# Kernel optimization log

Measured on AMD Instinct MI355X. Metric: run time of the kernel, lower is better.

Reference implementation:

```python
import jax, jax.numpy as jnp
import numpy as np

B, S, D, H, F = 2, 2048, 2048, 16, 8192
EPS = 1e-6


def _layernorm(x, g, b):
    # torch: mean/std over last dim, std is Bessel-corrected (unbiased), divide by (std + eps)
    m = jnp.mean(x, axis=-1, keepdims=True)
    s = jnp.std(x, axis=-1, keepdims=True, ddof=1)
    return g * (x - m) / (s + EPS) + b


def setup_inputs() -> dict:
    key = jax.random.key(0)
    ks = jax.random.split(key, 16)
    w = lambda k, shape, s=0.02: (jax.random.normal(k, shape, jnp.float32) * s)
    return {
        "x": jax.random.normal(ks[0], (B, S, D), jnp.float32),
        "mask": jnp.ones((1, 1, S, S), jnp.int32),
        "wq": w(ks[1], (D, D)), "bq": jnp.zeros((D,), jnp.float32),
        "wk": w(ks[2], (D, D)), "bk": jnp.zeros((D,), jnp.float32),
        "wv": w(ks[3], (D, D)), "bv": jnp.zeros((D,), jnp.float32),
        "wo": w(ks[4], (D, D)), "bo": jnp.zeros((D,), jnp.float32),
        "w1": w(ks[5], (D, F)), "b1": jnp.zeros((F,), jnp.float32),
        "w2": w(ks[6], (F, D)), "b2": jnp.zeros((D,), jnp.float32),
        "ln1_g": jnp.ones((D,), jnp.float32), "ln1_b": jnp.zeros((D,), jnp.float32),
        "ln2_g": jnp.ones((D,), jnp.float32), "ln2_b": jnp.zeros((D,), jnp.float32),
    }


def reference(x, mask, wq, bq, wk, bk, wv, bv, wo, bo, w1, b1, w2, b2, ln1_g, ln1_b, ln2_g, ln2_b):
    Bx, Sx, Dx = x.shape
    dk = Dx // H
    # --- self-attention sublayer (pre-norm residual) ---
    n = _layernorm(x, ln1_g, ln1_b)
    q = (n @ wq + bq).reshape(Bx, Sx, H, dk)
    k = (n @ wk + bk).reshape(Bx, Sx, H, dk)
    v = (n @ wv + bv).reshape(Bx, Sx, H, dk)
    scores = jnp.einsum('bqhd,bkhd->bhqk', q, k) / jnp.sqrt(jnp.float32(dk))
    scores = jnp.where(mask == 0, jnp.float32(-1e9), scores)
    attn = jax.nn.softmax(scores, axis=-1)  # [B,H,S,S]
    o = jnp.einsum('bhqk,bkhd->bqhd', attn, v).reshape(Bx, Sx, Dx)
    x = x + (o @ wo + bo)
    # --- feed-forward sublayer (pre-norm residual) ---
    n2 = _layernorm(x, ln2_g, ln2_b)
    x = x + (jax.nn.relu(n2 @ w1 + b1) @ w2 + b2)
    return x
```

## Files before the change

### kernel.cpp

```cpp
#include <hip/hip_runtime.h>
#include <hip/hip_bf16.h>
#include <cmath>

#define BB  2
#define SS  2048
#define DD  2048
#define HH  16
#define DKK 128
#define FF  8192
#define FQ  2048
#define MM  4096
#define EPSL 1e-6f

typedef __attribute__((ext_vector_type(8))) short  short8;
typedef __attribute__((ext_vector_type(4))) float  floatx4;
typedef __hip_bfloat16 bf16t;

__device__ __forceinline__ float bits2f(ushort u) {
    return __uint_as_float(((unsigned int)u) << 16);
}
__device__ __forceinline__ ushort f2bits(float f) {
    __hip_bfloat16 h = __float2bfloat16(f);
    return *reinterpret_cast<ushort*>(&h);
}

__global__ __launch_bounds__(256) void ln_kernel(const void* __restrict__ x,
                                                 const float* __restrict__ g,
                                                 const float* __restrict__ b,
                                                 bf16t* __restrict__ out,
                                                 int in_f32) {
    const int row = blockIdx.x;
    const int t = threadIdx.x;

    float v[8];
    if (in_f32) {
        const float* xr = (const float*)x + (size_t)row * DD;
        const float4 a4 = ((const float4*)xr)[2 * t];
        const float4 b4 = ((const float4*)xr)[2 * t + 1];
        v[0] = a4.x; v[1] = a4.y; v[2] = a4.z; v[3] = a4.w;
        v[4] = b4.x; v[5] = b4.y; v[6] = b4.z; v[7] = b4.w;
    } else {
        const ushort* xr = (const ushort*)x + (size_t)row * DD;
        union { uint4 u; ushort s[8]; } p;
        p.u = ((const uint4*)xr)[t];
#pragma unroll
        for (int i = 0; i < 8; i++) v[i] = bits2f(p.s[i]);
    }

    float sum = 0.f, sq = 0.f;
#pragma unroll
    for (int i = 0; i < 8; i++) { sum += v[i]; sq += v[i] * v[i]; }
#pragma unroll
    for (int off = 32; off > 0; off >>= 1) {
        sum += __shfl_down(sum, off);
        sq  += __shfl_down(sq, off);
    }
    __shared__ float ssum[4], ssq[4];
    const int wid = t >> 6, lane = t & 63;
    if (lane == 0) { ssum[wid] = sum; ssq[wid] = sq; }
    __syncthreads();
    if (t == 0) {
        float S = 0.f, Q = 0.f;
#pragma unroll
        for (int i = 0; i < 4; i++) { S += ssum[i]; Q += ssq[i]; }
        ssum[0] = S; ssq[0] = Q;
    }
    __syncthreads();
    const float S = ssum[0], Q = ssq[0];
    const float mean = S / (float)DD;
    float var = (Q - S * mean) / (float)(DD - 1);
    var = fmaxf(var, 0.f);
    const float inv = 1.0f / (sqrtf(var) + EPSL);

    const float4 ga = ((const float4*)g)[2 * t], gb = ((const float4*)g)[2 * t + 1];
    const float4 ba = ((const float4*)b)[2 * t], bb4 = ((const float4*)b)[2 * t + 1];
    const float gv[8] = {ga.x, ga.y, ga.z, ga.w, gb.x, gb.y, gb.z, gb.w};
    const float bv[8] = {ba.x, ba.y, ba.z, ba.w, bb4.x, bb4.y, bb4.z, bb4.w};

    union { uint4 u; ushort s[8]; } o;
#pragma unroll
    for (int i = 0; i < 8; i++) o.s[i] = f2bits((v[i] - mean) * inv * gv[i] + bv[i]);
    ((uint4*)((ushort*)out + (size_t)row * DD))[t] = o.u;
}

__global__ __launch_bounds__(256) void wtrans_kernel(const float* __restrict__ in,
                                                     bf16t* __restrict__ out,
                                                     int Cs, int r0, int c0, int nR) {
    __shared__ ushort tile[32][33];
    const int tx = threadIdx.x, ty = threadIdx.y;
    const int cc = blockIdx.x * 32, rr = blockIdx.y * 32;
#pragma unroll
    for (int j = 0; j < 4; j++)
        tile[ty + j * 8][tx] = f2bits(in[(size_t)(r0 + rr + ty + j * 8) * Cs + c0 + cc + tx]);
    __syncthreads();
    ushort* op = (ushort*)out;
#pragma unroll
    for (int j = 0; j < 4; j++)
        op[(size_t)(cc + ty + j * 8) * nR + rr + tx] = tile[tx][ty + j * 8];
}

__global__ __launch_bounds__(256) void gemm_bt(const bf16t* __restrict__ A,
                                               const bf16t* __restrict__ BT,
                                               const float* __restrict__ bias,
                                               const void* __restrict__ residual, int res_mode,
                                               void* __restrict__ C, int c_f32,
                                               int Nx, int Kx, int relu, int vt) {
    __shared__ __align__(16) ushort At[128 * 32];
    __shared__ __align__(16) ushort Bt[128 * 32];

    const int tid = threadIdx.x;
    const int wid = tid >> 6, lane = tid & 63;
    const int m16 = lane & 15, quad = lane >> 4;
    const int wr = wid >> 1, wc = wid & 1;
    const int m0 = blockIdx.y * 128, n0 = blockIdx.x * 128;

    floatx4 acc[4][4];
#pragma unroll
    for (int i = 0; i < 4; i++)
#pragma unroll
        for (int j = 0; j < 4; j++) acc[i][j] = (floatx4){0.f, 0.f, 0.f, 0.f};

    const int rc = lane >> 2, c8 = (lane & 3) * 8;
    const ushort* gA0 = (const ushort*)A  + (size_t)(m0 + rc) * Kx + c8;
    const ushort* gB0 = (const ushort*)BT + (size_t)(n0 + rc) * Kx + c8;

    const int nk = Kx / 32;
    for (int kt = 0; kt < nk; kt++) {
        __syncthreads();
#pragma unroll
        for (int cc = 0; cc < 2; cc++) {
            const int ch = wid * 2 + cc;
            const ushort* ga = gA0 + (size_t)(ch * 16) * Kx + kt * 32;
            const ushort* gb = gB0 + (size_t)(ch * 16) * Kx + kt * 32;
            __builtin_amdgcn_global_load_lds(
                (const __attribute__((address_space(1))) void*)ga,
                (__attribute__((address_space(3))) void*)(&At[ch * 512]), 16, 0, 0);
            __builtin_amdgcn_global_load_lds(
                (const __attribute__((address_space(1))) void*)gb,
                (__attribute__((address_space(3))) void*)(&Bt[ch * 512]), 16, 0, 0);
        }
        __syncthreads();

        short8 af[4], bfr[4];
#pragma unroll
        for (int i = 0; i < 4; i++)
            af[i] = *(const short8*)&At[(wr * 64 + i * 16 + m16) * 32 + quad * 8];
#pragma unroll
        for (int j = 0; j < 4; j++)
            bfr[j] = *(const short8*)&Bt[(wc * 64 + j * 16 + m16) * 32 + quad * 8];
#pragma unroll
        for (int i = 0; i < 4; i++)
#pragma unroll
            for (int j = 0; j < 4; j++)
                acc[i][j] = __builtin_amdgcn_mfma_f32_16x16x32_bf16(af[i], bfr[j], acc[i][j], 0, 0, 0);
    }

#pragma unroll
    for (int i = 0; i < 4; i++) {
        const int row = m0 + wr * 64 + i * 16 + quad * 4;
#pragma unroll
        for (int j = 0; j < 4; j++) {
            const int col = n0 + wc * 64 + j * 16 + m16;
            const float bb = bias ? bias[col] : 0.f;
#pragma unroll
            for (int r = 0; r < 4; r++) {
                float v = acc[i][j][r] + bb;
                if (vt) {
                    const int bb2 = (row + r) >> 11, s = (row + r) & 2047;
                    const int hh2 = col >> 7, dd2 = col & 127;
                    ((ushort*)C)[((size_t)(bb2 * HH + hh2) * DKK + dd2) * SS + s] = f2bits(v);
                } else {
                    const size_t idx = (size_t)(row + r) * Nx + col;
                    if (res_mode == 1)      v += ((const float*)residual)[idx];
                    else if (res_mode == 2) v += bits2f(((const ushort*)residual)[idx]);
                    if (relu) v = fmaxf(v, 0.f);
                    if (c_f32) ((float*)C)[idx] = v;
                    else       ((ushort*)C)[idx] = f2bits(v);
                }
            }
        }
    }
}

#define SQK 144
#define SV  72
#define SP  72
__global__ __launch_bounds__(256) void attn_kernel(const bf16t* __restrict__ q,
                                                   const bf16t* __restrict__ k,
                                                   const bf16t* __restrict__ vT,
                                                   bf16t* __restrict__ o) {
    __shared__ __align__(16) ushort Qt[64 * SQK];
    __shared__ __align__(16) ushort Kt[64 * SQK];
    __shared__ __align__(16) ushort Vt[128 * SV];
    __shared__ __align__(16) ushort Pt[4][16 * SP];

    const int tid = threadIdx.x;
    const int wid = tid >> 6, lane = tid & 63;
    const int m16 = lane & 15, quad = lane >> 4;
    const int qt = blockIdx.x, h = blockIdx.y, b = blockIdx.z;
    const int q0 = qt * 64;

    const ushort* qu = (const ushort*)q;
    const ushort* ku = (const ushort*)k;
    const ushort* vu = (const ushort*)vT;

#pragma unroll
    for (int it = 0; it < 4; it++) {
        const int c0 = tid + it * 256;
        const int r = c0 >> 4, cc = (c0 & 15) * 8;
        *(uint4*)&Qt[r * SQK + cc] =
            *(const uint4*)(qu + (size_t)(b * SS + q0 + r) * DD + h * DKK + cc);
    }

    float m_r[4], l_r[4];
    floatx4 acc_o[8];
#pragma unroll
    for (int r = 0; r < 4; r++) { m_r[r] = -1e30f; l_r[r] = 0.f; }
#pragma unroll
    for (int t = 0; t < 8; t++) acc_o[t] = (floatx4){0.f, 0.f, 0.f, 0.f};

    const float scale = 0.08838834764831845f;

    for (int kt2 = 0; kt2 < SS / 64; kt2++) {
        __syncthreads();
#pragma unroll
        for (int it = 0; it < 4; it++) {
            const int c0 = tid + it * 256;
            const int r = c0 >> 4, cc = (c0 & 15) * 8;
            *(uint4*)&Kt[r * SQK + cc] =
                *(const uint4*)(ku + (size_t)(b * SS + kt2 * 64 + r) * DD + h * DKK + cc);
            const int r2 = c0 >> 3, cc2 = (c0 & 7) * 8;
            *(uint4*)&Vt[r2 * SV + cc2] =
                *(const uint4*)(vu + (size_t)((b * HH + h) * DKK + r2) * SS + kt2 * 64 + cc2);
        }
        __syncthreads();

        short8 af[4];
#pragma unroll
        for (int kk = 0; kk < 4; kk++)
            af[kk] = *(const short8*)&Qt[(wid * 16 + m16) * SQK + kk * 32 + quad * 8];
        floatx4 sacc[4];
#pragma unroll
        for (int j = 0; j < 4; j++) {
            sacc[j] = (floatx4){0.f, 0.f, 0.f, 0.f};
#pragma unroll
            for (int kk = 0; kk < 4; kk++) {
                short8 bfk = *(const short8*)&Kt[(j * 16 + m16) * SQK + kk * 32 + quad * 8];
                sacc[j] = __builtin_amdgcn_mfma_f32_16x16x32_bf16(af[kk], bfk, sacc[j], 0, 0, 0);
            }
        }
#pragma unroll
        for (int r = 0; r < 4; r++) {
            float s0 = sacc[0][r] * scale, s1 = sacc[1][r] * scale;
            float s2 = sacc[2][r] * scale, s3 = sacc[3][r] * scale;
            float mx = fmaxf(fmaxf(s0, s1), fmaxf(s2, s3));
#pragma unroll
            for (int off = 1; off < 16; off <<= 1) mx = fmaxf(mx, __shfl_xor(mx, off));
            const float mnew = fmaxf(m_r[r], mx);
            const float alpha = __expf(m_r[r] - mnew);
            m_r[r] = mnew;
            const float p0 = __expf(s0 - mnew), p1 = __expf(s1 - mnew);
            const float p2 = __expf(s2 - mnew), p3 = __expf(s3 - mnew);
            float rs = p0 + p1 + p2 + p3;
#pragma unroll
            for (int off = 1; off < 16; off <<= 1) rs += __shfl_xor(rs, off);
            l_r[r] = l_r[r] * alpha + rs;
#pragma unroll
            for (int t = 0; t < 8; t++) acc_o[t][r] *= alpha;
            const int prow = (quad * 4 + r) * SP;
            Pt[wid][prow + 0 * 16 + m16] = f2bits(p0);
            Pt[wid][prow + 1 * 16 + m16] = f2bits(p1);
            Pt[wid][prow + 2 * 16 + m16] = f2bits(p2);
            Pt[wid][prow + 3 * 16 + m16] = f2bits(p3);
        }
#pragma unroll
        for (int kk2 = 0; kk2 < 2; kk2++) {
            short8 ap = *(const short8*)&Pt[wid][m16 * SP + kk2 * 32 + quad * 8];
#pragma unroll
            for (int t = 0; t < 8; t++) {
                short8 bv = *(const short8*)&Vt[(t * 16 + m16) * SV + kk2 * 32 + quad * 8];
                acc_o[t] = __builtin_amdgcn_mfma_f32_16x16x32_bf16(ap, bv, acc_o[t], 0, 0, 0);
            }
        }
    }

    ushort* ou = (ushort*)o;
#pragma unroll
    for (int t = 0; t < 8; t++) {
#pragma unroll
        for (int r = 0; r < 4; r++) {
            const float v = acc_o[t][r] / l_r[r];
            ou[(size_t)(b * SS + q0 + wid * 16 + quad * 4 + r) * DD + h * DKK + t * 16 + m16] = f2bits(v);
        }
    }
}

extern "C" void kernel_launch(void* const* d_in, const int* in_sizes, int n_in,
                              void* d_out, int out_size, void* d_ws, size_t ws_size,
                              hipStream_t stream) {
    const float* x   = (const float*)d_in[0];
    const float* wq = (const float*)d_in[2];  const float* bq = (const float*)d_in[3];
    const float* wk = (const float*)d_in[4];  const float* bk = (const float*)d_in[5];
    const float* wv = (const float*)d_in[6];  const float* bv = (const float*)d_in[7];
    const float* wo = (const float*)d_in[8];  const float* bo = (const float*)d_in[9];
    const float* w1 = (const float*)d_in[10]; const float* b1 = (const float*)d_in[11];
    const float* w2 = (const float*)d_in[12]; const float* b2 = (const float*)d_in[13];
    const float* g1 = (const float*)d_in[14]; const float* lb1 = (const float*)d_in[15];
    const float* g2 = (const float*)d_in[16]; const float* lb2 = (const float*)d_in[17];

    char* ws = (char*)d_ws;
    bf16t* S0 = (bf16t*)(ws);
    bf16t* S1 = (bf16t*)(ws + (16u << 20));
    bf16t* S2 = (bf16t*)(ws + (32u << 20));
    bf16t* S3 = (bf16t*)(ws + (48u << 20));
    bf16t* S2b = (bf16t*)(ws + (32u << 20) + (8u << 20));

    bf16t* n_buf  = S0;
    bf16t* k_buf  = S1;
    bf16t* wT_buf = S2;
    bf16t* vT_buf = S3;
    bf16t* q_buf  = (bf16t*)d_out;
    bf16t* a_buf  = S2;
    bf16t* woT    = S0;
    bf16t* x1_buf = S1;
    bf16t* n2_buf = S0;
    bf16t* w1Tq   = S2;
    bf16t* w2Tq   = S2b;
    bf16t* h_buf  = S3;

    const dim3 tb(32, 8);
    const dim3 grT(DD / 32, DD / 32);
    const dim3 grDD(DD / 128, MM / 128);

    ln_kernel<<<MM, 256, 0, stream>>>(x, g1, lb1, n_buf, 1);

    wtrans_kernel<<<grT, tb, 0, stream>>>(wq, wT_buf, DD, 0, 0, DD);
    gemm_bt<<<grDD, 256, 0, stream>>>(n_buf, wT_buf, bq, nullptr, 0, q_buf, 0, DD, DD, 0, 0);
    wtrans_kernel<<<grT, tb, 0, stream>>>(wk, wT_buf, DD, 0, 0, DD);
    gemm_bt<<<grDD, 256, 0, stream>>>(n_buf, wT_buf, bk, nullptr, 0, k_buf, 0, DD, DD, 0, 0);
    wtrans_kernel<<<grT, tb, 0, stream>>>(wv, wT_buf, DD, 0, 0, DD);
    gemm_bt<<<grDD, 256, 0, stream>>>(n_buf, wT_buf, bv, nullptr, 0, vT_buf, 0, DD, DD, 0, 1);

    attn_kernel<<<dim3(SS / 64, HH, BB), 256, 0, stream>>>(q_buf, k_buf, vT_buf, a_buf);

    wtrans_kernel<<<grT, tb, 0, stream>>>(wo, woT, DD, 0, 0, DD);
    gemm_bt<<<grDD, 256, 0, stream>>>(a_buf, woT, bo, x, 1, x1_buf, 0, DD, DD, 0, 0);

    ln_kernel<<<MM, 256, 0, stream>>>(x1_buf, g2, lb2, n2_buf, 0);

    for (int qtr = 0; qtr < 4; qtr++) {
        const int f0 = qtr * FQ;
        wtrans_kernel<<<dim3(FQ / 32, DD / 32), tb, 0, stream>>>(w1, w1Tq, FF, 0, f0, DD);
        gemm_bt<<<dim3(FQ / 128, MM / 128), 256, 0, stream>>>(
            n2_buf, w1Tq, b1 + f0, nullptr, 0, h_buf, 0, FQ, DD, 1, 0);
        wtrans_kernel<<<dim3(DD / 32, FQ / 32), tb, 0, stream>>>(w2, w2Tq, DD, f0, 0, FQ);
        gemm_bt<<<grDD, 256, 0, stream>>>(
            h_buf, w2Tq, qtr == 0 ? b2 : nullptr,
            qtr == 0 ? (const void*)x1_buf : (const void*)d_out, qtr == 0 ? 2 : 1,
            d_out, 1, DD, FQ, 0, 0);
    }
}
```

Before: 1.265 ms.

## Replace 128x128 GEMM with double-buffered 256x256 swizzled-LDS kernel, fuse K/V projections

Replaces the 128x128-tile, single-buffered GEMM with a 512-thread 256x256-tile kernel. It uses K=64 steps, XOR-swizzled LDS layout, double-buffered async global-to-LDS staging interleaved across eight MFMA phases, and raised wave priority around the MFMAs. It also fuses the K and V projections into one launch over a 4096-wide concatenated weight, keeps the residual stream in fp32 in the output buffer, and splits the FFN into halves instead of quarters. The aim is more data reuse per tile and overlap of loads with math, at the cost of higher register and LDS use. The larger tiles also produce fewer blocks per launch, which may underfill the GPU.

```diff
diff --git a/kernel.cpp b/kernel.cpp
--- a/kernel.cpp
+++ b/kernel.cpp
@@ -8,7 +8,7 @@
 #define HH  16
 #define DKK 128
 #define FF  8192
-#define FQ  2048
+#define FH  4096
 #define MM  4096
 #define EPSL 1e-6f
 
@@ -99,78 +99,137 @@
         op[(size_t)(cc + ty + j * 8) * nR + rr + tx] = tile[tx][ty + j * 8];
 }
 
-__global__ __launch_bounds__(256) void gemm_bt(const bf16t* __restrict__ A,
-                                               const bf16t* __restrict__ BT,
-                                               const float* __restrict__ bias,
-                                               const void* __restrict__ residual, int res_mode,
-                                               void* __restrict__ C, int c_f32,
-                                               int Nx, int Kx, int relu, int vt) {
-    __shared__ __align__(16) ushort At[128 * 32];
-    __shared__ __align__(16) ushort Bt[128 * 32];
+template<int IB>
+__device__ __forceinline__ void stage_half(const ushort* __restrict__ g, int Kx,
+                                           ushort* lds, int h, int wid, int lane) {
+#pragma unroll
+    for (int l = 0; l < 2; l++) {
+        const int c = wid * 2 + l;
+        const int rs = (IB == 6) ? (((c & 8) ? 128 : 0) + h * 64 + (c & 7) * 8)
+                                 : ((c >> 2) * 64 + h * 32 + (c & 3) * 8);
+        const int row = rs + (lane >> 3);
+        const int colb = ((lane & 7) * 16) ^ (((row >> 2) & 3) << 5);
+        const ushort* gp = g + (size_t)row * Kx + (colb >> 1);
+        __builtin_amdgcn_global_load_lds(
+            (const __attribute__((address_space(1))) void*)gp,
+            (__attribute__((address_space(3))) void*)(lds + rs * 64), 16, 0, 0);
+    }
+}
+
+#define VMCNT4 asm volatile("s_waitcnt vmcnt(4)" ::: "memory")
+#define VMCNT0 asm volatile("s_waitcnt vmcnt(0)" ::: "memory")
+
+#define STGA(buf, kt, h) stage_half<6>(gAu + (size_t)(kt) * 64, Kx, &LAf[(buf) * (256 * 64)], (h), wid, lane)
+#define STGB(buf, kt, h) stage_half<5>(gBu + (size_t)(kt) * 64, Kx, &LBf[(buf) * (256 * 64)], (h), wid, lane)
+
+#define PHASE(BUF, MH, NH, STAGE_STMT, WAIT_STMT)                                   \
+    do {                                                                            \
+        const ushort* LAc = &LAf[(BUF) * (256 * 64)];                               \
+        const ushort* LBc = &LBf[(BUF) * (256 * 64)];                               \
+        short8 af[4][2], bfr[2][2];                                                 \
+        _Pragma("unroll") for (int i = 0; i < 4; i++) {                             \
+            const int ar = arow0 + ((MH) * 4 + i) * 16;                             \
+            af[i][0] = *(const short8*)&LAc[ar * 64 + swz0];                        \
+            af[i][1] = *(const short8*)&LAc[ar * 64 + swz1];                        \
+        }                                                                           \
+        _Pragma("unroll") for (int j = 0; j < 2; j++) {                             \
+            const int br = brow0 + ((NH) * 2 + j) * 16;                             \
+            bfr[j][0] = *(const short8*)&LBc[br * 64 + swz0];                       \
+            bfr[j][1] = *(const short8*)&LBc[br * 64 + swz1];                       \
+        }                                                                           \
+        STAGE_STMT;                                                                 \
+        asm volatile("s_waitcnt lgkmcnt(8)" ::: "memory");                          \
+        __builtin_amdgcn_s_barrier();                                               \
+        asm volatile("s_waitcnt lgkmcnt(0)" ::: "memory");                          \
+        __builtin_amdgcn_s_setprio(1);                                              \
+        _Pragma("unroll") for (int i = 0; i < 4; i++)                               \
+            _Pragma("unroll") for (int j = 0; j < 2; j++) {                         \
+                acc[(MH) * 4 + i][(NH) * 2 + j] =                                   \
+                    __builtin_amdgcn_mfma_f32_16x16x32_bf16(                        \
+                        af[i][0], bfr[j][0], acc[(MH) * 4 + i][(NH) * 2 + j], 0, 0, 0); \
+                acc[(MH) * 4 + i][(NH) * 2 + j] =                                   \
+                    __builtin_amdgcn_mfma_f32_16x16x32_bf16(                        \
+                        af[i][1], bfr[j][1], acc[(MH) * 4 + i][(NH) * 2 + j], 0, 0, 0); \
+            }                                                                       \
+        __builtin_amdgcn_s_setprio(0);                                              \
+        WAIT_STMT;                                                                  \
+        __builtin_amdgcn_s_barrier();                                               \
+    } while (0)
+
+__global__ __launch_bounds__(512, 2) void gemm256(const bf16t* __restrict__ A,
+                                                  const bf16t* __restrict__ BT,
+                                                  const float* __restrict__ bias,
+                                                  const float* __restrict__ bias2,
+                                                  const void* __restrict__ residual, int res_mode,
+                                                  void* __restrict__ C, void* __restrict__ C2,
+                                                  int c_f32, int Nx, int Kx,
+                                                  int relu, int out_mode) {
+    __shared__ __align__(16) ushort LAf[2 * 256 * 64];
+    __shared__ __align__(16) ushort LBf[2 * 256 * 64];
 
     const int tid = threadIdx.x;
     const int wid = tid >> 6, lane = tid & 63;
     const int m16 = lane & 15, quad = lane >> 4;
-    const int wr = wid >> 1, wc = wid & 1;
-    const int m0 = blockIdx.y * 128, n0 = blockIdx.x * 128;
-
-    floatx4 acc[4][4];
-#pragma unroll
-    for (int i = 0; i < 4; i++)
+    const int wr = wid >> 2, wc = wid & 3;
+    const int m0 = blockIdx.y * 256, n0 = blockIdx.x * 256;
+
+    const ushort* gAu = (const ushort*)A + (size_t)m0 * Kx;
+    const ushort* gBu = (const ushort*)BT + (size_t)n0 * Kx;
+
+    floatx4 acc[8][4];
+#pragma unroll
+    for (int i = 0; i < 8; i++)
 #pragma unroll
         for (int j = 0; j < 4; j++) acc[i][j] = (floatx4){0.f, 0.f, 0.f, 0.f};
 
-    const int rc = lane >> 2, c8 = (lane & 3) * 8;
-    const ushort* gA0 = (const ushort*)A  + (size_t)(m0 + rc) * Kx + c8;
-    const ushort* gB0 = (const ushort*)BT + (size_t)(n0 + rc) * Kx + c8;
-
-    const int nk = Kx / 32;
-    for (int kt = 0; kt < nk; kt++) {
-        __syncthreads();
-#pragma unroll
-        for (int cc = 0; cc < 2; cc++) {
-            const int ch = wid * 2 + cc;
-            const ushort* ga = gA0 + (size_t)(ch * 16) * Kx + kt * 32;
-            const ushort* gb = gB0 + (size_t)(ch * 16) * Kx + kt * 32;
-            __builtin_amdgcn_global_load_lds(
-                (const __attribute__((address_space(1))) void*)ga,
-                (__attribute__((address_space(3))) void*)(&At[ch * 512]), 16, 0, 0);
-            __builtin_amdgcn_global_load_lds(
-                (const __attribute__((address_space(1))) void*)gb,
-                (__attribute__((address_space(3))) void*)(&Bt[ch * 512]), 16, 0, 0);
-        }
-        __syncthreads();
-
-        short8 af[4], bfr[4];
-#pragma unroll
-        for (int i = 0; i < 4; i++)
-            af[i] = *(const short8*)&At[(wr * 64 + i * 16 + m16) * 32 + quad * 8];
-#pragma unroll
-        for (int j = 0; j < 4; j++)
-            bfr[j] = *(const short8*)&Bt[(wc * 64 + j * 16 + m16) * 32 + quad * 8];
-#pragma unroll
-        for (int i = 0; i < 4; i++)
-#pragma unroll
-            for (int j = 0; j < 4; j++)
-                acc[i][j] = __builtin_amdgcn_mfma_f32_16x16x32_bf16(af[i], bfr[j], acc[i][j], 0, 0, 0);
-    }
-
-#pragma unroll
-    for (int i = 0; i < 4; i++) {
-        const int row = m0 + wr * 64 + i * 16 + quad * 4;
+    const int xsw = (m16 >> 2) & 3;
+    const int swz0 = (quad * 8) ^ (xsw << 4);
+    const int swz1 = (32 + quad * 8) ^ (xsw << 4);
+    const int arow0 = wr * 128 + m16;
+    const int brow0 = wc * 64 + m16;
+
+    const int nk = Kx / 64;
+
+    STGB(0, 0, 0); STGA(0, 0, 0); STGA(0, 0, 1); STGB(0, 0, 1);
+    STGB(1, 1, 0); STGA(1, 1, 0);
+    VMCNT4;
+    __builtin_amdgcn_s_barrier();
+
+    for (int t = 0; t < nk; t += 2) {
+        const bool pf = (t + 2 < nk);
+        PHASE(0, 0, 0, { STGA(1, t + 1, 1); }, {});
+        PHASE(0, 1, 0, { STGB(1, t + 1, 1); }, {});
+        PHASE(0, 0, 1, { if (pf) STGB(0, t + 2, 0); }, {});
+        PHASE(0, 1, 1, { if (pf) STGA(0, t + 2, 0); },
+              { if (pf) { VMCNT4; } else { VMCNT0; } });
+        PHASE(1, 0, 0, { if (pf) STGA(0, t + 2, 1); }, {});
+        PHASE(1, 1, 0, { if (pf) STGB(0, t + 2, 1); }, {});
+        PHASE(1, 0, 1, { if (pf) STGB(1, t + 3, 0); }, {});
+        PHASE(1, 1, 1, { if (pf) STGA(1, t + 3, 0); },
+              { if (pf) { VMCNT4; } });
+    }
+
+#pragma unroll
+    for (int i = 0; i < 8; i++) {
+        const int row = m0 + wr * 128 + i * 16 + quad * 4;
 #pragma unroll
         for (int j = 0; j < 4; j++) {
             const int col = n0 + wc * 64 + j * 16 + m16;
-            const float bb = bias ? bias[col] : 0.f;
+            const bool isv = (out_mode == 1) || (out_mode == 2 && col >= DD);
+            const int cv = (out_mode == 2 && col >= DD) ? col - DD : col;
+            const float bb = (out_mode == 2 && col >= DD)
+                                 ? bias2[cv]
+                                 : (bias ? bias[col] : 0.f);
 #pragma unroll
             for (int r = 0; r < 4; r++) {
                 float v = acc[i][j][r] + bb;
-                if (vt) {
+                if (isv) {
                     const int bb2 = (row + r) >> 11, s = (row + r) & 2047;
-                    const int hh2 = col >> 7, dd2 = col & 127;
-                    ((ushort*)C)[((size_t)(bb2 * HH + hh2) * DKK + dd2) * SS + s] = f2bits(v);
+                    const int hh2 = cv >> 7, dd2 = cv & 127;
+                    ushort* dst = (ushort*)((out_mode == 2) ? C2 : C);
+                    dst[((size_t)(bb2 * HH + hh2) * DKK + dd2) * SS + s] = f2bits(v);
                 } else {
-                    const size_t idx = (size_t)(row + r) * Nx + col;
+                    const size_t idx = (size_t)(row + r) * Nx + cv;
                     if (res_mode == 1)      v += ((const float*)residual)[idx];
                     else if (res_mode == 2) v += bits2f(((const ushort*)residual)[idx]);
                     if (relu) v = fmaxf(v, 0.f);
@@ -313,7 +372,6 @@
     bf16t* S1 = (bf16t*)(ws + (16u << 20));
     bf16t* S2 = (bf16t*)(ws + (32u << 20));
     bf16t* S3 = (bf16t*)(ws + (48u << 20));
-    bf16t* S2b = (bf16t*)(ws + (32u << 20) + (8u << 20));
 
     bf16t* n_buf  = S0;
     bf16t* k_buf  = S1;
@@ -322,41 +380,42 @@
     bf16t* q_buf  = (bf16t*)d_out;
     bf16t* a_buf  = S2;
     bf16t* woT    = S0;
-    bf16t* x1_buf = S1;
     bf16t* n2_buf = S0;
-    bf16t* w1Tq   = S2;
-    bf16t* w2Tq   = S2b;
-    bf16t* h_buf  = S3;
+    bf16t* h_buf  = S1;
+    bf16t* wfT    = S3;
 
     const dim3 tb(32, 8);
     const dim3 grT(DD / 32, DD / 32);
-    const dim3 grDD(DD / 128, MM / 128);
+    const dim3 gr256(DD / 256, MM / 256);
+    const dim3 grKV(2 * DD / 256, MM / 256);
 
     ln_kernel<<<MM, 256, 0, stream>>>(x, g1, lb1, n_buf, 1);
 
     wtrans_kernel<<<grT, tb, 0, stream>>>(wq, wT_buf, DD, 0, 0, DD);
-    gemm_bt<<<grDD, 256, 0, stream>>>(n_buf, wT_buf, bq, nullptr, 0, q_buf, 0, DD, DD, 0, 0);
+    gemm256<<<gr256, 512, 0, stream>>>(n_buf, wT_buf, bq, nullptr, nullptr, 0,
+                                       q_buf, nullptr, 0, DD, DD, 0, 0);
+
     wtrans_kernel<<<grT, tb, 0, stream>>>(wk, wT_buf, DD, 0, 0, DD);
-    gemm_bt<<<grDD, 256, 0, stream>>>(n_buf, wT_buf, bk, nullptr, 0, k_buf, 0, DD, DD, 0, 0);
-    wtrans_kernel<<<grT, tb, 0, stream>>>(wv, wT_buf, DD, 0, 0, DD);
-    gemm_bt<<<grDD, 256, 0, stream>>>(n_buf, wT_buf, bv, nullptr, 0, vT_buf, 0, DD, DD, 0, 1);
+    wtrans_kernel<<<grT, tb, 0, stream>>>(wv, wT_buf + (size_t)DD * DD, DD, 0, 0, DD);
+    gemm256<<<grKV, 512, 0, stream>>>(n_buf, wT_buf, bk, bv, nullptr, 0,
+                                      k_buf, vT_buf, 0, DD, DD, 0, 2);
 
     attn_kernel<<<dim3(SS / 64, HH, BB), 256, 0, stream>>>(q_buf, k_buf, vT_buf, a_buf);
 
     wtrans_kernel<<<grT, tb, 0, stream>>>(wo, woT, DD, 0, 0, DD);
-    gemm_bt<<<grDD, 256, 0, stream>>>(a_buf, woT, bo, x, 1, x1_buf, 0, DD, DD, 0, 0);
-
-    ln_kernel<<<MM, 256, 0, stream>>>(x1_buf, g2, lb2, n2_buf, 0);
-
-    for (int qtr = 0; qtr < 4; qtr++) {
-        const int f0 = qtr * FQ;
-        wtrans_kernel<<<dim3(FQ / 32, DD / 32), tb, 0, stream>>>(w1, w1Tq, FF, 0, f0, DD);
-        gemm_bt<<<dim3(FQ / 128, MM / 128), 256, 0, stream>>>(
-            n2_buf, w1Tq, b1 + f0, nullptr, 0, h_buf, 0, FQ, DD, 1, 0);
-        wtrans_kernel<<<dim3(DD / 32, FQ / 32), tb, 0, stream>>>(w2, w2Tq, DD, f0, 0, FQ);
-        gemm_bt<<<grDD, 256, 0, stream>>>(
-            h_buf, w2Tq, qtr == 0 ? b2 : nullptr,
-            qtr == 0 ? (const void*)x1_buf : (const void*)d_out, qtr == 0 ? 2 : 1,
-            d_out, 1, DD, FQ, 0, 0);
-    }
-}
+    gemm256<<<gr256, 512, 0, stream>>>(a_buf, woT, bo, nullptr, x, 1,
+                                       d_out, nullptr, 1, DD, DD, 0, 0);
+
+    ln_kernel<<<MM, 256, 0, stream>>>(d_out, g2, lb2, n2_buf, 1);
+
+    for (int hf = 0; hf < 2; hf++) {
+        const int f0 = hf * FH;
+        wtrans_kernel<<<dim3(FH / 32, DD / 32), tb, 0, stream>>>(w1, wfT, FF, 0, f0, DD);
+        gemm256<<<dim3(FH / 256, MM / 256), 512, 0, stream>>>(
+            n2_buf, wfT, b1 + f0, nullptr, nullptr, 0, h_buf, nullptr, 0, FH, DD, 1, 0);
+        wtrans_kernel<<<dim3(DD / 32, FH / 32), tb, 0, stream>>>(w2, wfT, DD, f0, 0, FH);
+        gemm256<<<gr256, 512, 0, stream>>>(
+            h_buf, wfT, hf == 0 ? b2 : nullptr, nullptr, d_out, 1,
+            d_out, nullptr, 1, DD, FH, 0, 0);
+    }
+}
```

Measured after the change: 1.406 ms. 11.1% more time.
